# Optimization experiments

Measured on AMD Instinct MI355X. Metric: run time of the kernel, lower is better.

## Reference

```python
import jax, jax.numpy as jnp
import numpy as np

NUM_USERS = 100000
NUM_ITEMS = 50000
N_NODES = NUM_USERS + NUM_ITEMS
LATENT_DIM = 64
SBERT_DIM = 384
NUM_LAYERS = 3
N_EDGES = 2_000_000


def setup_inputs() -> dict:
    key = jax.random.key(0)
    k1, k2, k3, k4 = jax.random.split(key, 4)
    edge_index = jax.random.randint(k1, (2, N_EDGES), 0, N_NODES, dtype=jnp.int32)
    user_emb = jax.random.normal(k2, (NUM_USERS, LATENT_DIM), dtype=jnp.float32) * 0.1
    book_bert = jax.random.normal(k3, (NUM_ITEMS, SBERT_DIM), dtype=jnp.float32)
    # torch Linear weight layout: [out_features, in_features]
    w_proj = jax.random.normal(k4, (LATENT_DIM, SBERT_DIM), dtype=jnp.float32) * (1.0 / np.sqrt(SBERT_DIM))
    return {"edge_index": edge_index, "user_emb": user_emb, "book_bert": book_bert, "w_proj": w_proj}


def reference(edge_index, user_emb, book_bert, w_proj):
    src, dst = edge_index[0], edge_index[1]
    # initial embeddings: [users ; proj(book_bert)] -> [N, D]
    book_emb = book_bert @ w_proj.T
    emb0 = jnp.concatenate([user_emb, book_emb], axis=0)

    # symmetric gcn_norm without self-loops (PyG LGConv default)
    ones = jnp.ones((src.shape[0],), dtype=emb0.dtype)
    deg = jax.ops.segment_sum(ones, dst, num_segments=N_NODES)
    dis = jnp.where(deg > 0, jax.lax.rsqrt(jnp.maximum(deg, 1.0)), 0.0)
    norm = dis[src] * dis[dst]  # [E]

    x = emb0
    acc = emb0
    for _ in range(NUM_LAYERS):
        # out[dst] += norm * x[src]  (gather-scatter SpMM)
        msgs = norm[:, None] * x[src]  # [E, D]
        x = jax.ops.segment_sum(msgs, dst, num_segments=N_NODES)
        acc = acc + x
    out = acc / jnp.asarray(NUM_LAYERS + 1, dtype=emb0.dtype)
    return (emb0, out)
```

## Files before the change

kernel.cpp:

```cpp
#include <hip/hip_runtime.h>
#include <hip/hip_bf16.h>
#include <stdint.h>

#define NUM_USERS 100000
#define NUM_ITEMS 50000
#define N_NODES   150000
#define LATENT    64
#define SBERT     384
#define N_EDGES   2000000
#define OUT_OFF   (N_NODES * LATENT)
#define NBUCK     586
#define BCAP      4096
#define EPB       8192

typedef __hip_bfloat16 bf16;

__device__ __forceinline__ int ufl(int v) { return __builtin_amdgcn_readfirstlane(v); }

__global__ void k_zero_bcnt(int* __restrict__ bcnt) {
    int i = blockIdx.x * 256 + threadIdx.x;
    if (i < NBUCK) bcnt[i] = 0;
}

__global__ __launch_bounds__(256) void k_bin(const int* __restrict__ src,
                                             const int* __restrict__ dst,
                                             int* __restrict__ bcnt,
                                             unsigned* __restrict__ bin) {
    __shared__ int hist[NBUCK];
    __shared__ int base[NBUCK];
    const int tid = threadIdx.x;
    for (int i = tid; i < NBUCK; i += 256) hist[i] = 0;
    __syncthreads();
    const int e0 = blockIdx.x * EPB;
    const int e1 = min(e0 + EPB, N_EDGES);
    for (int e = e0 + tid; e < e1; e += 256)
        atomicAdd(&hist[dst[e] >> 8], 1);
    __syncthreads();
    for (int i = tid; i < NBUCK; i += 256) {
        int c = hist[i];
        base[i] = c ? atomicAdd(&bcnt[i], c) : 0;
        hist[i] = 0;
    }
    __syncthreads();
    for (int e = e0 + tid; e < e1; e += 256) {
        int d = dst[e];
        int b = d >> 8;
        int p = base[b] + atomicAdd(&hist[b], 1);
        bin[(size_t)b * BCAP + p] = (unsigned)src[e] | ((unsigned)(d & 255) << 18);
    }
}

__global__ __launch_bounds__(1024) void k_bscan(const int* __restrict__ bcnt,
                                                int* __restrict__ bbase) {
    __shared__ int sm[1024];
    int tid = threadIdx.x;
    int v = (tid < NBUCK) ? bcnt[tid] : 0;
    sm[tid] = v;
    __syncthreads();
    for (int off = 1; off < 1024; off <<= 1) {
        int t = (tid >= off) ? sm[tid - off] : 0;
        __syncthreads();
        sm[tid] += t;
        __syncthreads();
    }
    if (tid <= NBUCK) bbase[tid] = (tid == 0) ? 0 : sm[tid - 1];
}

__global__ __launch_bounds__(256) void k_build(const unsigned* __restrict__ bin,
                                               const int* __restrict__ bcnt,
                                               const int* __restrict__ bbase,
                                               int* __restrict__ rp,
                                               float* __restrict__ dis,
                                               int* __restrict__ cws) {
    __shared__ int h[256];
    __shared__ int lc[256];
    const int tid   = threadIdx.x;
    const int b     = blockIdx.x;
    const int nbase = b << 8;
    const unsigned* mybin = bin + (size_t)b * BCAP;
    h[tid] = 0;
    __syncthreads();
    const int cnt  = bcnt[b];
    const int base = bbase[b];
    for (int i = tid; i < cnt; i += 256)
        atomicAdd(&h[mybin[i] >> 18], 1);
    __syncthreads();
    int v = h[tid];
    __shared__ int sm[256];
    sm[tid] = v;
    __syncthreads();
    for (int off = 1; off < 256; off <<= 1) {
        int t = (tid >= off) ? sm[tid - off] : 0;
        __syncthreads();
        sm[tid] += t;
        __syncthreads();
    }
    int excl = sm[tid] - v;
    int n = nbase + tid;
    if (n < N_NODES) {
        rp[n]  = base + excl;
        dis[n] = (v > 0) ? rsqrtf((float)v) : 0.0f;
    }
    lc[tid] = base + excl;
    if (b == NBUCK - 1 && tid == 0) rp[N_NODES] = N_EDGES;
    __syncthreads();
    for (int i = tid; i < cnt; i += 256) {
        unsigned rec = mybin[i];
        int dl = rec >> 18;
        int pos = atomicAdd(&lc[dl], 1);
        cws[pos] = (int)(rec & 0x3FFFF);
    }
}

__global__ void k_copy_user(const float* __restrict__ u, const float* __restrict__ dis,
                            float* __restrict__ out, bf16* __restrict__ y) {
    int i = blockIdx.x * 256 + threadIdx.x;
    if (i < NUM_USERS * LATENT) {
        float v = u[i];
        out[i] = v;
        out[OUT_OFF + i] = v;
        float d = dis[i >> 6];
        y[i] = __float2bfloat16(d * v);
    }
}

__global__ __launch_bounds__(256) void k_proj(const float* __restrict__ bert,
                                              const float* __restrict__ w,
                                              const float* __restrict__ dis,
                                              float* __restrict__ out,
                                              bf16* __restrict__ y) {
    __shared__ float sB[128][33];
    __shared__ float sW[32][64];
    const int tid  = threadIdx.x;
    const int rb   = blockIdx.x * 128;
    const int col8 = (tid & 7) * 8;
    const int rowg = (tid >> 3) * 4;

    float acc[4][8];
#pragma unroll
    for (int i = 0; i < 4; ++i)
#pragma unroll
        for (int j = 0; j < 8; ++j) acc[i][j] = 0.0f;

    for (int kb = 0; kb < SBERT; kb += 32) {
        __syncthreads();
#pragma unroll
        for (int j = 0; j < 4; ++j) {
            int idx = tid + j * 256;
            int r  = idx >> 3;
            int k4 = (idx & 7) * 4;
            int rr = min(rb + r, NUM_ITEMS - 1);
            float4 v = *(const float4*)(bert + (size_t)rr * SBERT + kb + k4);
            sB[r][k4 + 0] = v.x; sB[r][k4 + 1] = v.y;
            sB[r][k4 + 2] = v.z; sB[r][k4 + 3] = v.w;
        }
#pragma unroll
        for (int j = 0; j < 2; ++j) {
            int idx = tid + j * 256;
            int c  = idx >> 3;
            int k4 = (idx & 7) * 4;
            float4 v = *(const float4*)(w + (size_t)c * SBERT + kb + k4);
            sW[k4 + 0][c] = v.x; sW[k4 + 1][c] = v.y;
            sW[k4 + 2][c] = v.z; sW[k4 + 3][c] = v.w;
        }
        __syncthreads();
#pragma unroll
        for (int kk = 0; kk < 32; ++kk) {
            float4 w0 = *(const float4*)&sW[kk][col8];
            float4 w1 = *(const float4*)&sW[kk][col8 + 4];
#pragma unroll
            for (int i = 0; i < 4; ++i) {
                float a = sB[rowg + i][kk];
                acc[i][0] = fmaf(a, w0.x, acc[i][0]);
                acc[i][1] = fmaf(a, w0.y, acc[i][1]);
                acc[i][2] = fmaf(a, w0.z, acc[i][2]);
                acc[i][3] = fmaf(a, w0.w, acc[i][3]);
                acc[i][4] = fmaf(a, w1.x, acc[i][4]);
                acc[i][5] = fmaf(a, w1.y, acc[i][5]);
                acc[i][6] = fmaf(a, w1.z, acc[i][6]);
                acc[i][7] = fmaf(a, w1.w, acc[i][7]);
            }
        }
    }
#pragma unroll
    for (int i = 0; i < 4; ++i) {
        int r = rb + rowg + i;
        if (r < NUM_ITEMS) {
            int n = NUM_USERS + r;
            size_t o = (size_t)n * LATENT + col8;
            float d = dis[n];
            float4 f0 = make_float4(acc[i][0], acc[i][1], acc[i][2], acc[i][3]);
            float4 f1 = make_float4(acc[i][4], acc[i][5], acc[i][6], acc[i][7]);
            *(float4*)(out + o)           = f0;
            *(float4*)(out + o + 4)       = f1;
            *(float4*)(out + OUT_OFF + o) = f0;
            *(float4*)(out + OUT_OFF + o + 4) = f1;
#pragma unroll
            for (int j = 0; j < 8; ++j) y[o + j] = __float2bfloat16(d * acc[i][j]);
        }
    }
}

template <bool FINAL>
__global__ __launch_bounds__(256) void k_spmm(const bf16* __restrict__ y,
                                              const int* __restrict__ rp,
                                              const int* __restrict__ cws,
                                              const float* __restrict__ dis,
                                              bf16* __restrict__ yn,
                                              float* __restrict__ acc) {
    int lane = threadIdx.x & 63;
    int node = ufl(blockIdx.x * 4 + (threadIdx.x >> 6));
    int beg = rp[node];
    int end = rp[node + 1];
    int last = end - 1;
    float a = 0.0f;
    for (int base = beg; base < end; base += 8) {
        int idx[8];
#pragma unroll
        for (int j = 0; j < 8; ++j)
            idx[j] = cws[min(base + j, last)];
        float v[8];
#pragma unroll
        for (int j = 0; j < 8; ++j)
            v[j] = __bfloat162float(y[(size_t)idx[j] * LATENT + lane]);
#pragma unroll
        for (int j = 0; j < 8; ++j)
            if (base + j <= last) a += v[j];
    }
    float d = dis[node];
    size_t o = (size_t)node * LATENT + lane;
    if (!FINAL) yn[o] = __float2bfloat16(d * d * a);
    float t = acc[o] + d * a;
    acc[o] = FINAL ? t * 0.25f : t;
}

extern "C" void kernel_launch(void* const* d_in, const int* in_sizes, int n_in,
                              void* d_out, int out_size, void* d_ws, size_t ws_size,
                              hipStream_t stream) {
    const int*   ei    = (const int*)d_in[0];
    const float* uemb  = (const float*)d_in[1];
    const float* bert  = (const float*)d_in[2];
    const float* wproj = (const float*)d_in[3];
    float* out = (float*)d_out;

    char* ws = (char*)d_ws;
    size_t off = 0;
    auto carve = [&](size_t bytes) -> void* {
        void* p = ws + off;
        off += (bytes + 255) & ~(size_t)255;
        return p;
    };
    float*    dis    = (float*)carve(sizeof(float) * N_NODES);
    int*      rp     = (int*)carve(sizeof(int) * (N_NODES + 1));
    int*      bcnt   = (int*)carve(sizeof(int) * NBUCK);
    int*      bbase  = (int*)carve(sizeof(int) * (NBUCK + 1));
    unsigned* bin    = (unsigned*)carve(sizeof(unsigned) * (size_t)NBUCK * BCAP);
    int*      cws    = (int*)carve(sizeof(int) * N_EDGES);
    bf16*     ye     = (bf16*)carve(sizeof(bf16) * (size_t)N_NODES * LATENT);
    bf16*     y0     = (bf16*)carve(sizeof(bf16) * (size_t)N_NODES * LATENT);
    bf16*     y1     = (bf16*)carve(sizeof(bf16) * (size_t)N_NODES * LATENT);

    const int* srcI = ei;
    const int* dstI = ei + N_EDGES;

    k_zero_bcnt<<<(NBUCK + 255) / 256, 256, 0, stream>>>(bcnt);
    k_bin<<<(N_EDGES + EPB - 1) / EPB, 256, 0, stream>>>(srcI, dstI, bcnt, bin);
    k_bscan<<<1, 1024, 0, stream>>>(bcnt, bbase);
    k_build<<<NBUCK, 256, 0, stream>>>(bin, bcnt, bbase, rp, dis, cws);
    k_copy_user<<<(NUM_USERS * LATENT + 255) / 256, 256, 0, stream>>>(uemb, dis, out, ye);
    k_proj<<<(NUM_ITEMS + 127) / 128, 256, 0, stream>>>(bert, wproj, dis, out, ye);

    float* accp = out + OUT_OFF;
    k_spmm<false><<<N_NODES / 4, 256, 0, stream>>>(ye, rp, cws, dis, y0, accp);
    k_spmm<false><<<N_NODES / 4, 256, 0, stream>>>(y0, rp, cws, dis, y1, accp);
    k_spmm<true ><<<N_NODES / 4, 256, 0, stream>>>(y1, rp, cws, dis, y0, accp);
}
```

Measured before the change: 463.6 us.

## Use nontemporal loads/stores, register-cache edges in binning, hoist SpMM acc load

The binning kernel now processes half as many edges per block and keeps each thread's 16 edge records in registers, so src/dst are read once instead of twice. Streaming global loads and stores across binning, build, copy, projection and SpMM are marked nontemporal to reduce cache pollution. The SpMM kernel loads the accumulator before the gather loop so its latency overlaps the neighbour reads. Splitting float4 stores into scalar nontemporal stores may cost store efficiency, and the smaller blocks add more global atomics on bucket counts.

```diff
diff --git a/kernel.cpp b/kernel.cpp
--- a/kernel.cpp
+++ b/kernel.cpp
@@ -11,11 +11,16 @@
 #define OUT_OFF   (N_NODES * LATENT)
 #define NBUCK     586
 #define BCAP      4096
-#define EPB       8192
+#define EPB       4096
 
 typedef __hip_bfloat16 bf16;
 
 __device__ __forceinline__ int ufl(int v) { return __builtin_amdgcn_readfirstlane(v); }
+
+__device__ __forceinline__ void nt_store_bf16(bf16* p, bf16 v) {
+    __builtin_nontemporal_store(*reinterpret_cast<unsigned short*>(&v),
+                                reinterpret_cast<unsigned short*>(p));
+}
 
 __global__ void k_zero_bcnt(int* __restrict__ bcnt) {
     int i = blockIdx.x * 256 + threadIdx.x;
@@ -30,11 +35,26 @@
     __shared__ int base[NBUCK];
     const int tid = threadIdx.x;
     for (int i = tid; i < NBUCK; i += 256) hist[i] = 0;
-    __syncthreads();
     const int e0 = blockIdx.x * EPB;
-    const int e1 = min(e0 + EPB, N_EDGES);
-    for (int e = e0 + tid; e < e1; e += 256)
-        atomicAdd(&hist[dst[e] >> 8], 1);
+
+    unsigned rec[16];
+    int bb[16];
+#pragma unroll
+    for (int j = 0; j < 16; ++j) {
+        int e = e0 + tid + j * 256;
+        if (e < N_EDGES) {
+            int d = __builtin_nontemporal_load(dst + e);
+            int s = __builtin_nontemporal_load(src + e);
+            bb[j]  = d >> 8;
+            rec[j] = (unsigned)s | ((unsigned)(d & 255) << 18);
+        } else {
+            bb[j] = -1;
+        }
+    }
+    __syncthreads();
+#pragma unroll
+    for (int j = 0; j < 16; ++j)
+        if (bb[j] >= 0) atomicAdd(&hist[bb[j]], 1);
     __syncthreads();
     for (int i = tid; i < NBUCK; i += 256) {
         int c = hist[i];
@@ -42,12 +62,14 @@
         hist[i] = 0;
     }
     __syncthreads();
-    for (int e = e0 + tid; e < e1; e += 256) {
-        int d = dst[e];
-        int b = d >> 8;
-        int p = base[b] + atomicAdd(&hist[b], 1);
-        bin[(size_t)b * BCAP + p] = (unsigned)src[e] | ((unsigned)(d & 255) << 18);
-    }
+    int p[16];
+#pragma unroll
+    for (int j = 0; j < 16; ++j)
+        if (bb[j] >= 0) p[j] = atomicAdd(&hist[bb[j]], 1);
+#pragma unroll
+    for (int j = 0; j < 16; ++j)
+        if (bb[j] >= 0)
+            bin[(size_t)bb[j] * BCAP + base[bb[j]] + p[j]] = rec[j];
 }
 
 __global__ __launch_bounds__(1024) void k_bscan(const int* __restrict__ bcnt,
@@ -83,7 +105,7 @@
     const int cnt  = bcnt[b];
     const int base = bbase[b];
     for (int i = tid; i < cnt; i += 256)
-        atomicAdd(&h[mybin[i] >> 18], 1);
+        atomicAdd(&h[__builtin_nontemporal_load(mybin + i) >> 18], 1);
     __syncthreads();
     int v = h[tid];
     __shared__ int sm[256];
@@ -105,7 +127,7 @@
     if (b == NBUCK - 1 && tid == 0) rp[N_NODES] = N_EDGES;
     __syncthreads();
     for (int i = tid; i < cnt; i += 256) {
-        unsigned rec = mybin[i];
+        unsigned rec = __builtin_nontemporal_load(mybin + i);
         int dl = rec >> 18;
         int pos = atomicAdd(&lc[dl], 1);
         cws[pos] = (int)(rec & 0x3FFFF);
@@ -116,9 +138,9 @@
                             float* __restrict__ out, bf16* __restrict__ y) {
     int i = blockIdx.x * 256 + threadIdx.x;
     if (i < NUM_USERS * LATENT) {
-        float v = u[i];
-        out[i] = v;
-        out[OUT_OFF + i] = v;
+        float v = __builtin_nontemporal_load(u + i);
+        __builtin_nontemporal_store(v, out + i);
+        __builtin_nontemporal_store(v, out + OUT_OFF + i);
         float d = dis[i >> 6];
         y[i] = __float2bfloat16(d * v);
     }
@@ -150,7 +172,11 @@
             int r  = idx >> 3;
             int k4 = (idx & 7) * 4;
             int rr = min(rb + r, NUM_ITEMS - 1);
-            float4 v = *(const float4*)(bert + (size_t)rr * SBERT + kb + k4);
+            const float* bp = bert + (size_t)rr * SBERT + kb + k4;
+            float4 v = make_float4(__builtin_nontemporal_load(bp + 0),
+                                   __builtin_nontemporal_load(bp + 1),
+                                   __builtin_nontemporal_load(bp + 2),
+                                   __builtin_nontemporal_load(bp + 3));
             sB[r][k4 + 0] = v.x; sB[r][k4 + 1] = v.y;
             sB[r][k4 + 2] = v.z; sB[r][k4 + 3] = v.w;
         }
@@ -189,14 +215,12 @@
             int n = NUM_USERS + r;
             size_t o = (size_t)n * LATENT + col8;
             float d = dis[n];
-            float4 f0 = make_float4(acc[i][0], acc[i][1], acc[i][2], acc[i][3]);
-            float4 f1 = make_float4(acc[i][4], acc[i][5], acc[i][6], acc[i][7]);
-            *(float4*)(out + o)           = f0;
-            *(float4*)(out + o + 4)       = f1;
-            *(float4*)(out + OUT_OFF + o) = f0;
-            *(float4*)(out + OUT_OFF + o + 4) = f1;
-#pragma unroll
-            for (int j = 0; j < 8; ++j) y[o + j] = __float2bfloat16(d * acc[i][j]);
+#pragma unroll
+            for (int j = 0; j < 8; ++j) {
+                __builtin_nontemporal_store(acc[i][j], out + o + j);
+                __builtin_nontemporal_store(acc[i][j], out + OUT_OFF + o + j);
+                y[o + j] = __float2bfloat16(d * acc[i][j]);
+            }
         }
     }
 }
@@ -213,6 +237,9 @@
     int beg = rp[node];
     int end = rp[node + 1];
     int last = end - 1;
+    float d = dis[node];
+    size_t o = (size_t)node * LATENT + lane;
+    float accv = acc[o];
     float a = 0.0f;
     for (int base = beg; base < end; base += 8) {
         int idx[8];
@@ -227,11 +254,10 @@
         for (int j = 0; j < 8; ++j)
             if (base + j <= last) a += v[j];
     }
-    float d = dis[node];
-    size_t o = (size_t)node * LATENT + lane;
-    if (!FINAL) yn[o] = __float2bfloat16(d * d * a);
-    float t = acc[o] + d * a;
-    acc[o] = FINAL ? t * 0.25f : t;
+    if (!FINAL)
+        nt_store_bf16(yn + o, __float2bfloat16(d * d * a));
+    float t = accv + d * a;
+    __builtin_nontemporal_store(FINAL ? t * 0.25f : t, acc + o);
 }
 
 extern "C" void kernel_launch(void* const* d_in, const int* in_sizes, int n_in,
```

Measured after the change: 454.6 us. No clear change (-1.9%).
